# Performance work log

Measured on AMD Instinct MI355X. Metric: run time of the kernel, lower is better.

## Reference

```python
import jax, jax.numpy as jnp
import numpy as np

K = 1024   # in_dim = out_dim = per-head dim (module uses full k per head)
H = 4      # heads
B, T = 2, 2048


def setup_inputs() -> dict:
    key = jax.random.key(0)
    ks = jax.random.split(key, 7)
    s = 0.02
    return {
        "x": jax.random.normal(ks[0], (B, T, K), jnp.float32),
        "Wq": jax.random.normal(ks[1], (K, K * H), jnp.float32) * s,
        "Wk": jax.random.normal(ks[2], (K, K * H), jnp.float32) * s,
        "Wv": jax.random.normal(ks[3], (K, K * H), jnp.float32) * s,
        "Wu": jax.random.normal(ks[4], (K * H, K), jnp.float32) * s,
        "bu": jnp.zeros((K,), jnp.float32),
        "W1": jax.random.normal(ks[5], (K, K), jnp.float32) * s,
        "b1": jnp.zeros((K,), jnp.float32),
        "W2": jax.random.normal(ks[6], (K, K), jnp.float32) * s,
        "b2": jnp.zeros((K,), jnp.float32),
    }


def reference(x, Wq, Wk, Wv, Wu, bu, W1, b1, W2, b2):
    b, t, k = x.shape
    h = H
    scale = k ** (-0.25)
    # projections: each head gets FULL dim k (quirk of the original module)
    q = (x @ Wq).reshape(b, t, h, k) * scale   # [b,t,h,k]
    kk = (x @ Wk).reshape(b, t, h, k) * scale
    v = (x @ Wv).reshape(b, t, h, k)
    # attention scores [b,h,q,k_pos]
    dot = jnp.einsum("bqhd,bkhd->bhqk", q, kk)
    causal = jnp.tril(jnp.ones((t, t), bool))  # strictly-upper masked to -inf
    dot = jnp.where(causal, dot, -jnp.inf)
    attn = jax.nn.softmax(dot, axis=-1)
    out = jnp.einsum("bhqk,bkhd->bqhd", attn, v).reshape(b, t, h * k)
    attn_out = out @ Wu + bu                   # unifyheads
    x = x + attn_out                            # residual
    ff = jax.nn.relu(x @ W1 + b1) @ W2 + b2     # in_dim == out_dim
    return x + ff                               # residual around FFN
```

## Files before the change

### kernel.cpp

```cpp
#include <hip/hip_runtime.h>
#include <math.h>


#define TM 128
#define TN 128
#define BK 64

typedef __attribute__((ext_vector_type(8))) short short8;
typedef __attribute__((ext_vector_type(4))) float f32x4;

__device__ __forceinline__ unsigned short f2bf(float f) {
  union { float f; unsigned int u; } v; v.f = f;
  unsigned int r = (v.u + 0x7fffu + ((v.u >> 16) & 1u)) >> 16;
  return (unsigned short)r;
}
__device__ __forceinline__ float bf2f(unsigned short b) {
  union { unsigned int u; float f; } v; v.u = ((unsigned int)b) << 16;
  return v.f;
}

#define GL2LDS(g, l)                                                          \
  __builtin_amdgcn_global_load_lds(                                           \
      (__attribute__((address_space(1))) void*)(g),                           \
      (__attribute__((address_space(3))) void*)(l), 16, 0, 0)

__device__ __forceinline__ void gemm_core(
    const unsigned short* __restrict__ A, const unsigned short* __restrict__ BT,
    int m0, int n0, int kmax, int lda, int ldb, int ldc, long long coff,
    float scale, const float* __restrict__ bias,
    const float* __restrict__ resid, int do_relu, float* __restrict__ Cf,
    unsigned short* __restrict__ Cb, unsigned short* As, unsigned short* Bs) {
  const int tid = threadIdx.x;
  const int lane = tid & 63;
  const int wv = tid >> 6;
  const int wm = wv & 1;
  const int wn = wv >> 1;

  const int srow = tid >> 2;
  const int scol = (tid & 3) * 8;
  const unsigned short* ap0 = A + (long long)(m0 + srow) * lda + scol;
  const unsigned short* ap1 = ap0 + (long long)64 * lda;
  const unsigned short* bp0 = BT + (long long)(n0 + srow) * ldb + scol;
  const unsigned short* bp1 = bp0 + (long long)64 * ldb;
  unsigned short* lA00 = As + wv * 512;
  unsigned short* lA10 = As + 2048 + wv * 512;
  unsigned short* lA01 = As + 4096 + wv * 512;
  unsigned short* lA11 = As + 6144 + wv * 512;
  unsigned short* lB00 = Bs + wv * 512;
  unsigned short* lB10 = Bs + 2048 + wv * 512;
  unsigned short* lB01 = Bs + 4096 + wv * 512;
  unsigned short* lB11 = Bs + 6144 + wv * 512;

  f32x4 acc[4][4];
#pragma unroll
  for (int i = 0; i < 4; ++i)
#pragma unroll
    for (int j2 = 0; j2 < 4; ++j2) acc[i][j2] = {0.f, 0.f, 0.f, 0.f};

  const int frow = lane & 15;
  const int fq = (lane >> 4) * 8;

  for (int k0 = 0; k0 < kmax; k0 += BK) {
    __syncthreads();
    GL2LDS(ap0, lA00); GL2LDS(ap0 + 32, lA01);
    GL2LDS(ap1, lA10); GL2LDS(ap1 + 32, lA11);
    GL2LDS(bp0, lB00); GL2LDS(bp0 + 32, lB01);
    GL2LDS(bp1, lB10); GL2LDS(bp1 + 32, lB11);
    ap0 += BK; ap1 += BK; bp0 += BK; bp1 += BK;
    __syncthreads();

#pragma unroll
    for (int s = 0; s < 2; ++s) {
      short8 afr[4], bfr[4];
#pragma unroll
      for (int mi = 0; mi < 4; ++mi)
        afr[mi] = *(const short8*)(As + s * 4096 +
                                   (wm * 64 + mi * 16 + frow) * 32 + fq);
#pragma unroll
      for (int ni = 0; ni < 4; ++ni)
        bfr[ni] = *(const short8*)(Bs + s * 4096 +
                                   (wn * 64 + ni * 16 + frow) * 32 + fq);
#pragma unroll
      for (int mi = 0; mi < 4; ++mi)
#pragma unroll
        for (int ni = 0; ni < 4; ++ni)
          acc[mi][ni] = __builtin_amdgcn_mfma_f32_16x16x32_bf16(
              afr[mi], bfr[ni], acc[mi][ni], 0, 0, 0);
    }
  }

  const int ccol = lane & 15;
  const int crow = (lane >> 4) * 4;
#pragma unroll
  for (int mi = 0; mi < 4; ++mi) {
#pragma unroll
    for (int ni = 0; ni < 4; ++ni) {
      const int gc = n0 + wn * 64 + ni * 16 + ccol;
#pragma unroll
      for (int r = 0; r < 4; ++r) {
        const int gr = m0 + wm * 64 + mi * 16 + crow + r;
        float v = acc[mi][ni][r] * scale;
        if (bias) v += bias[gc];
        if (resid) v += resid[(long long)gr * ldc + gc];
        if (do_relu) v = fmaxf(v, 0.f);
        const long long ci = coff + (long long)gr * ldc + gc;
        if (Cf) Cf[ci] = v;
        if (Cb) Cb[ci] = f2bf(v);
      }
    }
  }
}

__global__ __launch_bounds__(256) void gemm_bt(
    const unsigned short* __restrict__ A, const unsigned short* __restrict__ BT,
    int Kd, int lda, int ldb, int ldc, int bh_shift,
    long long aob, long long aoh, long long bob, long long boh,
    long long cob, long long coh, float scale,
    const float* __restrict__ bias, const float* __restrict__ resid,
    int do_relu, float* __restrict__ Cf, unsigned short* __restrict__ Cb,
    int causal_mode, int grid_mode) {
  __shared__ unsigned short As[8192];
  __shared__ unsigned short Bs[8192];
  int n0, m0, z;
  if (grid_mode == 2) {
    z = blockIdx.x; n0 = blockIdx.y * TN; m0 = blockIdx.z * TM;
  } else if (grid_mode == 4) {
    z = blockIdx.x; m0 = blockIdx.y * TM; n0 = blockIdx.z * TN;
  } else if (grid_mode == 6) {
    const int bid = blockIdx.x;
    const int xcd = bid & 7;
    const int j = bid >> 3;
    const int ns = j >> 2;
    m0 = (xcd * 4 + (j & 3)) * TM;
    n0 = (ns >> 2) * TN;
    z = ns & 3;
  } else {
    n0 = blockIdx.x * TN; m0 = blockIdx.y * TM; z = blockIdx.z;
  }

  const int zb = z >> bh_shift;
  const int zh = z & ((1 << bh_shift) - 1);
  const long long aoff = (long long)zb * aob + (long long)zh * aoh;
  const long long boff = (long long)zb * bob + (long long)zh * boh;
  const long long coff = (long long)zb * cob + (long long)zh * coh;

  int kmax = Kd;
  if (causal_mode == 2) { int t = m0 + TM; if (t < kmax) kmax = t; }

  gemm_core(A + aoff, BT + boff, m0, n0, kmax, lda, ldb, ldc, coff, scale,
            bias, resid, do_relu, Cf, Cb, As, Bs);
}

__global__ __launch_bounds__(256) void gemm_t(
    const unsigned short* __restrict__ xb,
    const unsigned short* __restrict__ Wcomb,
    unsigned short* __restrict__ tb) {
  __shared__ unsigned short As[8192];
  __shared__ unsigned short Bs[8192];
  const int bid = blockIdx.x;
  const int xcd = bid & 7;
  const int j = bid >> 3;
  const int m0 = (xcd * 4 + (j & 3)) * TM;
  const int n0 = (j >> 2) * TN;
  gemm_core(xb, Wcomb, m0, n0, 1024, 1024, 1024, 4096, 0, 1.0f,
            nullptr, nullptr, 0, nullptr, tb, As, Bs);
}

__global__ __launch_bounds__(256) void gemm_sv(
    const unsigned short* __restrict__ xb,
    const unsigned short* __restrict__ Wcomb,
    const unsigned short* __restrict__ tb,
    unsigned short* __restrict__ S, unsigned short* __restrict__ vT) {
  __shared__ unsigned short As[8192];
  __shared__ unsigned short Bs[8192];
  const long long TT = (long long)2048 * 2048;
  const int bid = blockIdx.x;
  if (bid < 1088) {
    const int z = bid & 7, zb = z >> 2, zh = z & 3;
    const int idx = bid >> 3;
    int m = (int)((sqrtf(8.0f * idx + 1.0f) - 1.0f) * 0.5f);
    while ((m + 1) * (m + 2) / 2 <= idx) ++m;
    while (m * (m + 1) / 2 > idx) --m;
    const int m0 = m * TM;
    const int n0 = (idx - m * (m + 1) / 2) * TN;
    gemm_core(tb + (long long)zb * 2048 * 4096 + zh * 1024,
              xb + (long long)zb * 2048 * 1024,
              m0, n0, 1024, 4096, 1024, 2048,
              (long long)zb * 4 * TT + (long long)zh * TT,
              1.0f, nullptr, nullptr, 0, nullptr, S, As, Bs);
  } else {
    const int r = bid - 1088;
    const int xcd = r & 7;
    const int j = r >> 3;
    const int bb = j >> 6;
    const int rr = j & 63;
    const int m0 = (xcd * 4 + (rr & 3)) * TM;
    const int n0 = (rr >> 2) * TN;
    gemm_core(Wcomb + (size_t)4096 * 1024, xb + (long long)bb * 2048 * 1024,
              m0, n0, 1024, 1024, 1024, 2048, (long long)bb * 4096 * 2048,
              1.0f, nullptr, nullptr, 0, nullptr, vT, As, Bs);
  }
}

__global__ __launch_bounds__(256) void reduce_epi(
    const unsigned short* __restrict__ Pb, int S, long long MN,
    const float* __restrict__ bias, const float* __restrict__ resid,
    int do_relu, float* __restrict__ Cf, unsigned short* __restrict__ Cb) {
  const long long i4 = ((long long)blockIdx.x * 256 + threadIdx.x) * 4;
  if (i4 >= MN) return;
  float4 s = {0.f, 0.f, 0.f, 0.f};
  for (int t = 0; t < S; ++t) {
    const ushort4 p = *(const ushort4*)(Pb + (long long)t * MN + i4);
    s.x += bf2f(p.x); s.y += bf2f(p.y); s.z += bf2f(p.z); s.w += bf2f(p.w);
  }
  if (bias) {
    const int c0 = (int)(i4 & 1023);
    s.x += bias[c0]; s.y += bias[c0 + 1]; s.z += bias[c0 + 2]; s.w += bias[c0 + 3];
  }
  if (resid) {
    const float4 rr = *(const float4*)(resid + i4);
    s.x += rr.x; s.y += rr.y; s.z += rr.z; s.w += rr.w;
  }
  if (do_relu) {
    s.x = fmaxf(s.x, 0.f); s.y = fmaxf(s.y, 0.f);
    s.z = fmaxf(s.z, 0.f); s.w = fmaxf(s.w, 0.f);
  }
  if (Cf) *(float4*)(Cf + i4) = s;
  if (Cb) {
    ushort4 o;
    o.x = f2bf(s.x); o.y = f2bf(s.y); o.z = f2bf(s.z); o.w = f2bf(s.w);
    *(ushort4*)(Cb + i4) = o;
  }
}

__global__ __launch_bounds__(256) void softmax_causal(unsigned short* S, int T) {
  const int q = blockIdx.x;
  unsigned short* row = S + ((long long)blockIdx.y * T + q) * T;
  const int tid = threadIdx.x;
  const int lane = tid & 63;
  const int wv = tid >> 6;
  const int n = q + 1;
  const int nz = (n + 127) & ~127;
  const int base = tid * 8;
  short8 raw = {};
  if (base < nz) raw = *(const short8*)(row + base);
  float vals[8];
  float m = -__builtin_inff();
#pragma unroll
  for (int i = 0; i < 8; ++i) {
    vals[i] = (base + i < n) ? bf2f((unsigned short)raw[i]) : -__builtin_inff();
    m = fmaxf(m, vals[i]);
  }
#pragma unroll
  for (int o = 32; o; o >>= 1) m = fmaxf(m, __shfl_xor(m, o, 64));
  __shared__ float red[4];
  if (lane == 0) red[wv] = m;
  __syncthreads();
  m = fmaxf(fmaxf(red[0], red[1]), fmaxf(red[2], red[3]));
  __syncthreads();
  float s = 0.f, e[8];
#pragma unroll
  for (int i = 0; i < 8; ++i) {
    e[i] = (base + i < n) ? __expf(vals[i] - m) : 0.f;
    s += e[i];
  }
#pragma unroll
  for (int o = 32; o; o >>= 1) s += __shfl_xor(s, o, 64);
  if (lane == 0) red[wv] = s;
  __syncthreads();
  s = red[0] + red[1] + red[2] + red[3];
  const float inv = 1.f / s;
  if (base < nz) {
    short8 o8;
#pragma unroll
    for (int i = 0; i < 8; ++i) o8[i] = (short)f2bf(e[i] * inv);
    *(short8*)(row + base) = o8;
  }
}

__global__ __launch_bounds__(256) void prep_all(
    const float* __restrict__ x, const float* __restrict__ Wq,
    const float* __restrict__ Wk, const float* __restrict__ Wv,
    const float* __restrict__ Wu, const float* __restrict__ W1,
    const float* __restrict__ W2, unsigned short* __restrict__ xb,
    unsigned short* __restrict__ Wqc, unsigned short* __restrict__ Wkc,
    unsigned short* __restrict__ Wvc, unsigned short* __restrict__ WuTb,
    unsigned short* __restrict__ W1T, unsigned short* __restrict__ W2T,
    float s2) {
  const int z = blockIdx.y;
  if (z <= 3) {
    const float* src = (z == 0) ? x : (z == 1) ? Wq : (z == 2) ? Wk : Wv;
    unsigned short* dst = (z == 0) ? xb : (z == 1) ? Wqc : (z == 2) ? Wkc : Wvc;
    const float sc = (z == 2) ? s2 : 1.0f;
    const long long i4 = ((long long)blockIdx.x * 256 + threadIdx.x) * 4;
    const float4 v = *(const float4*)(src + i4);
    ushort4 u;
    u.x = f2bf(v.x * sc); u.y = f2bf(v.y * sc);
    u.z = f2bf(v.z * sc); u.w = f2bf(v.w * sc);
    *(ushort4*)(dst + i4) = u;
    return;
  }
  const int R = (z == 4) ? 4096 : 1024;
  const int by = blockIdx.x >> 5;
  if (by * 32 >= R) return;
  const float* W = (z == 4) ? Wu : (z == 5) ? W1 : W2;
  unsigned short* WT = (z == 4) ? WuTb : (z == 5) ? W1T : W2T;
  __shared__ float tile[32][33];
  const int c0 = (blockIdx.x & 31) * 32;
  const int r0 = by * 32;
  const int tx = threadIdx.x & 31;
  const int ty = threadIdx.x >> 5;
#pragma unroll
  for (int j = 0; j < 32; j += 8)
    tile[ty + j][tx] = W[(long long)(r0 + ty + j) * 1024 + c0 + tx];
  __syncthreads();
#pragma unroll
  for (int j = 0; j < 32; j += 8)
    WT[(long long)(c0 + ty + j) * R + r0 + tx] = f2bf(tile[tx][ty + j]);
}

extern "C" void kernel_launch(void* const* d_in, const int* in_sizes, int n_in,
                              void* d_out, int out_size, void* d_ws,
                              size_t ws_size, hipStream_t stream) {
  (void)in_sizes; (void)n_in; (void)out_size; (void)ws_size;
  const float* x  = (const float*)d_in[0];
  const float* Wq = (const float*)d_in[1];
  const float* Wk = (const float*)d_in[2];
  const float* Wv = (const float*)d_in[3];
  const float* Wu = (const float*)d_in[4];
  const float* bu = (const float*)d_in[5];
  const float* W1 = (const float*)d_in[6];
  const float* b1 = (const float*)d_in[7];
  const float* W2 = (const float*)d_in[8];
  const float* b2 = (const float*)d_in[9];
  float* out = (float*)d_out;

  const int T = 2048, K = 1024;
  const int BT = 4096;
  const size_t MB = 1024 * 1024;
  const long long MN = (long long)BT * K;
  const long long TT = (long long)T * T;
  const long long Mi = 1024 * 1024;

  char* w = (char*)d_ws;
  unsigned short* xb    = (unsigned short*)(w + 0 * MB);
  unsigned short* Wqc   = (unsigned short*)(w + 8 * MB);
  unsigned short* Wvc   = (unsigned short*)(w + 16 * MB);
  unsigned short* Wkc   = (unsigned short*)(w + 24 * MB);
  unsigned short* WuTb  = (unsigned short*)(w + 32 * MB);
  unsigned short* Wcomb = (unsigned short*)(w + 40 * MB);
  unsigned short* tb    = (unsigned short*)(w + 56 * MB);
  unsigned short* vT    = (unsigned short*)(w + 88 * MB);
  unsigned short* S     = (unsigned short*)(w + 120 * MB);
  unsigned short* W1T   = (unsigned short*)(w + 184 * MB);
  unsigned short* W2T   = (unsigned short*)(w + 186 * MB);
  unsigned short* Pb    = (unsigned short*)(w + 40 * MB);
  float*          x1f   = (float*)(w + 8 * MB);
  unsigned short* x1b   = (unsigned short*)(w + 24 * MB);
  unsigned short* h1    = (unsigned short*)(w + 32 * MB);
  unsigned short* Pb2   = (unsigned short*)(w + 88 * MB);

  const float s2 = 0.03125f;

  prep_all<<<dim3(4096, 7), 256, 0, stream>>>(
      x, Wq, Wk, Wv, Wu, W1, W2, xb, Wqc, Wkc, Wvc, WuTb, W1T, W2T, s2);

  gemm_bt<<<dim3(8, 8, 8), 256, 0, stream>>>(
      Wkc, Wqc, K, 4096, 4096, 1024, 2,
      4 * Mi, 1024, 4 * Mi, 1024, 4 * Mi, Mi, 1.0f,
      nullptr, nullptr, 0, nullptr, Wcomb, 0, 2);

  gemm_t<<<dim3(1024), 256, 0, stream>>>(xb, Wcomb, tb);

  gemm_sv<<<dim3(2112), 256, 0, stream>>>(xb, Wcomb, tb, S, vT);

  softmax_causal<<<dim3(T, 8), 256, 0, stream>>>(S, T);

  gemm_bt<<<dim3(8, T / TM, K / TN), 256, 0, stream>>>(
      S, vT, T, T, 2048, K, 2,
      (long long)4 * TT, TT, (long long)4096 * 2048, (long long)1024 * 2048,
      (long long)2048 * 1024, MN, 1.0f,
      nullptr, nullptr, 0, nullptr, Pb, 2, 4);

  reduce_epi<<<dim3(4096), 256, 0, stream>>>(Pb, 4, MN, bu, x, 0, x1f, x1b);

  gemm_bt<<<dim3(1024), 256, 0, stream>>>(
      x1b, W1T, 256, K, K, K, 0,
      256, 0, 256, 0, MN, 0, 1.0f,
      nullptr, nullptr, 0, nullptr, Pb2, 0, 6);
  reduce_epi<<<dim3(4096), 256, 0, stream>>>(Pb2, 4, MN, b1, nullptr, 1,
                                             nullptr, h1);

  gemm_bt<<<dim3(1024), 256, 0, stream>>>(
      h1, W2T, 256, K, K, K, 0,
      256, 0, 256, 0, MN, 0, 1.0f,
      nullptr, nullptr, 0, nullptr, Pb2, 0, 6);
  reduce_epi<<<dim3(4096), 256, 0, stream>>>(Pb2, 4, MN, b2, x1f, 0, out,
                                             nullptr);
}
```

Before: 486.7 us.

## Replace split-K FFN GEMMs and reduce passes with fused 128x64 full-K GEMM

The two FFN matmuls previously ran as split-K (4 slices of 256) into bf16 partial buffers, each followed by a reduce_epi pass that applied bias, relu and residual. The new gemm_ffn kernel uses 128x64 tiles over the full K=1024 with 512 blocks and an XCD-aware block mapping, and applies bias, relu and residual directly in its epilogue. This removes two launches and the write/read of the partial buffers, and accumulates in fp32 instead of summing bf16 partials. The cost is fewer blocks with longer K loops and no double-buffering, which may lower latency hiding.

```diff
diff --git a/kernel.cpp b/kernel.cpp
--- a/kernel.cpp
+++ b/kernel.cpp
@@ -104,6 +104,97 @@
         if (resid) v += resid[(long long)gr * ldc + gc];
         if (do_relu) v = fmaxf(v, 0.f);
         const long long ci = coff + (long long)gr * ldc + gc;
+        if (Cf) Cf[ci] = v;
+        if (Cb) Cb[ci] = f2bf(v);
+      }
+    }
+  }
+}
+
+__device__ __forceinline__ void core64(
+    f32x4 acc[4][2], const unsigned short* __restrict__ A, int lda,
+    const unsigned short* __restrict__ BT, int ldb, int kmax,
+    unsigned short* As, unsigned short* Bs) {
+  const int tid = threadIdx.x;
+  const int lane = tid & 63;
+  const int wv = tid >> 6;
+  const int wm = wv & 1;
+  const int wn = wv >> 1;
+  const int srow = tid >> 2;
+  const int scol = (tid & 3) * 8;
+  const unsigned short* ap0 = A + (long long)srow * lda + scol;
+  const unsigned short* ap1 = ap0 + (long long)64 * lda;
+  const unsigned short* bp0 = BT + (long long)srow * ldb + scol;
+  unsigned short* lA00 = As + wv * 512;
+  unsigned short* lA10 = As + 2048 + wv * 512;
+  unsigned short* lA01 = As + 4096 + wv * 512;
+  unsigned short* lA11 = As + 6144 + wv * 512;
+  unsigned short* lB00 = Bs + wv * 512;
+  unsigned short* lB01 = Bs + 2048 + wv * 512;
+  const int frow = lane & 15;
+  const int fq = (lane >> 4) * 8;
+  for (int k0 = 0; k0 < kmax; k0 += 64) {
+    __syncthreads();
+    GL2LDS(ap0, lA00); GL2LDS(ap0 + 32, lA01);
+    GL2LDS(ap1, lA10); GL2LDS(ap1 + 32, lA11);
+    GL2LDS(bp0, lB00); GL2LDS(bp0 + 32, lB01);
+    ap0 += 64; ap1 += 64; bp0 += 64;
+    __syncthreads();
+#pragma unroll
+    for (int s = 0; s < 2; ++s) {
+      short8 afr[4], bfr[2];
+#pragma unroll
+      for (int mi = 0; mi < 4; ++mi)
+        afr[mi] = *(const short8*)(As + s * 4096 +
+                                   (wm * 64 + mi * 16 + frow) * 32 + fq);
+#pragma unroll
+      for (int ni = 0; ni < 2; ++ni)
+        bfr[ni] = *(const short8*)(Bs + s * 2048 +
+                                   (wn * 32 + ni * 16 + frow) * 32 + fq);
+#pragma unroll
+      for (int mi = 0; mi < 4; ++mi)
+#pragma unroll
+        for (int ni = 0; ni < 2; ++ni)
+          acc[mi][ni] = __builtin_amdgcn_mfma_f32_16x16x32_bf16(
+              afr[mi], bfr[ni], acc[mi][ni], 0, 0, 0);
+    }
+  }
+}
+
+__global__ __launch_bounds__(256) void gemm_ffn(
+    const unsigned short* __restrict__ A, const unsigned short* __restrict__ BT,
+    const float* __restrict__ bias, const float* __restrict__ resid,
+    int do_relu, float* __restrict__ Cf, unsigned short* __restrict__ Cb) {
+  __shared__ unsigned short As[8192];
+  __shared__ unsigned short Bs[4096];
+  const int bid = blockIdx.x;
+  const int xcd = bid & 7;
+  const int j = bid >> 3;
+  const int m0 = (xcd * 4 + (j & 3)) * 128;
+  const int n0 = (j >> 2) * 64;
+  f32x4 acc[4][2];
+#pragma unroll
+  for (int i = 0; i < 4; ++i)
+#pragma unroll
+    for (int j2 = 0; j2 < 2; ++j2) acc[i][j2] = {0.f, 0.f, 0.f, 0.f};
+  core64(acc, A + (long long)m0 * 1024, 1024, BT + (long long)n0 * 1024, 1024,
+         1024, As, Bs);
+  const int lane = threadIdx.x & 63;
+  const int wv = threadIdx.x >> 6;
+  const int wm = wv & 1, wn = wv >> 1;
+  const int ccol = lane & 15, crow = (lane >> 4) * 4;
+#pragma unroll
+  for (int mi = 0; mi < 4; ++mi) {
+#pragma unroll
+    for (int ni = 0; ni < 2; ++ni) {
+      const int gc = n0 + wn * 32 + ni * 16 + ccol;
+#pragma unroll
+      for (int r = 0; r < 4; ++r) {
+        const int gr = m0 + wm * 64 + mi * 16 + crow + r;
+        float v = acc[mi][ni][r] + bias[gc];
+        if (resid) v += resid[(long long)gr * 1024 + gc];
+        if (do_relu) v = fmaxf(v, 0.f);
+        const long long ci = (long long)gr * 1024 + gc;
         if (Cf) Cf[ci] = v;
         if (Cb) Cb[ci] = f2bf(v);
       }
@@ -126,14 +217,6 @@
     z = blockIdx.x; n0 = blockIdx.y * TN; m0 = blockIdx.z * TM;
   } else if (grid_mode == 4) {
     z = blockIdx.x; m0 = blockIdx.y * TM; n0 = blockIdx.z * TN;
-  } else if (grid_mode == 6) {
-    const int bid = blockIdx.x;
-    const int xcd = bid & 7;
-    const int j = bid >> 3;
-    const int ns = j >> 2;
-    m0 = (xcd * 4 + (j & 3)) * TM;
-    n0 = (ns >> 2) * TN;
-    z = ns & 3;
   } else {
     n0 = blockIdx.x * TN; m0 = blockIdx.y * TM; z = blockIdx.z;
   }
@@ -336,9 +419,8 @@
   float* out = (float*)d_out;
 
   const int T = 2048, K = 1024;
-  const int BT = 4096;
   const size_t MB = 1024 * 1024;
-  const long long MN = (long long)BT * K;
+  const long long MN = (long long)4096 * 1024;
   const long long TT = (long long)T * T;
   const long long Mi = 1024 * 1024;
 
@@ -358,7 +440,6 @@
   float*          x1f   = (float*)(w + 8 * MB);
   unsigned short* x1b   = (unsigned short*)(w + 24 * MB);
   unsigned short* h1    = (unsigned short*)(w + 32 * MB);
-  unsigned short* Pb2   = (unsigned short*)(w + 88 * MB);
 
   const float s2 = 0.03125f;
 
@@ -384,17 +465,8 @@
 
   reduce_epi<<<dim3(4096), 256, 0, stream>>>(Pb, 4, MN, bu, x, 0, x1f, x1b);
 
-  gemm_bt<<<dim3(1024), 256, 0, stream>>>(
-      x1b, W1T, 256, K, K, K, 0,
-      256, 0, 256, 0, MN, 0, 1.0f,
-      nullptr, nullptr, 0, nullptr, Pb2, 0, 6);
-  reduce_epi<<<dim3(4096), 256, 0, stream>>>(Pb2, 4, MN, b1, nullptr, 1,
-                                             nullptr, h1);
-
-  gemm_bt<<<dim3(1024), 256, 0, stream>>>(
-      h1, W2T, 256, K, K, K, 0,
-      256, 0, 256, 0, MN, 0, 1.0f,
-      nullptr, nullptr, 0, nullptr, Pb2, 0, 6);
-  reduce_epi<<<dim3(4096), 256, 0, stream>>>(Pb2, 4, MN, b2, x1f, 0, out,
-                                             nullptr);
-}
+  gemm_ffn<<<dim3(512), 256, 0, stream>>>(x1b, W1T, b1, nullptr, 1,
+                                          nullptr, h1);
+
+  gemm_ffn<<<dim3(512), 256, 0, stream>>>(h1, W2T, b2, x1f, 0, out, nullptr);
+}
```

Measured after the change: 452.3 us. -7.1%, faster.
